# Performance work log

Measured on AMD Instinct MI355X. Metric: run time of the kernel, lower is better.

The kernel has to match this reference:

```python
import jax, jax.numpy as jnp
import numpy as np

DIM = 256
NUM_HEADS = 8
SAMPLE_RATIO = 4
B, H, W = 8, 32, 32
HEAD_DIM = DIM // NUM_HEADS
SCALE = HEAD_DIM ** (-0.5)


def conv1x1(x, w, b):
    # x: [B,C,H,W], w: [O,C], b: [O]  (1x1 conv == per-pixel channel matmul)
    return jnp.einsum('bchw,oc->bohw', x, w) + b[None, :, None, None]


def setup_inputs() -> dict:
    key = jax.random.key(0)
    ks = jax.random.split(key, 16)
    s = 0.02
    x = jax.random.normal(ks[0], (B, DIM, H, W), dtype=jnp.float32)
    # gumbel noise for the two gumbel-softmax gates (sampled once, fed as input)
    u_q = jax.random.uniform(ks[1], (B, SAMPLE_RATIO, H, W), minval=1e-6, maxval=1.0 - 1e-6)
    u_k = jax.random.uniform(ks[2], (B, SAMPLE_RATIO, H, W), minval=1e-6, maxval=1.0 - 1e-6)
    g_q = -jnp.log(-jnp.log(u_q))
    g_k = -jnp.log(-jnp.log(u_k))
    return {
        'x': x,
        'g_q': g_q,
        'g_k': g_k,
        'Wsq': jax.random.normal(ks[3], (SAMPLE_RATIO, DIM)) * s,
        'bsq': jnp.zeros((SAMPLE_RATIO,), jnp.float32),
        'Wsk': jax.random.normal(ks[4], (SAMPLE_RATIO, DIM)) * s,
        'bsk': jnp.zeros((SAMPLE_RATIO,), jnp.float32),
        'Wq': jax.random.normal(ks[5], (DIM, DIM)) * s,
        'bq': jnp.zeros((DIM,), jnp.float32),
        'Wk': jax.random.normal(ks[6], (DIM, DIM)) * s,
        'bk': jnp.zeros((DIM,), jnp.float32),
        'Wv': jax.random.normal(ks[7], (DIM, DIM)) * s,
        'bv': jnp.zeros((DIM,), jnp.float32),
        'Wp': jax.random.normal(ks[8], (DIM, DIM)) * s,
        'bp': jnp.zeros((DIM,), jnp.float32),
    }


def reference(x, g_q, g_k, Wsq, bsq, Wsk, bsk, Wq, bq, Wk, bk, Wv, bv, Wp, bp):
    Bn, C, Hh, Ww = x.shape
    N = Hh * Ww
    # gumbel-softmax (soft, tau=1) gates; keep channel 0 only
    sample_q = jax.nn.softmax(conv1x1(x, Wsq, bsq) + g_q, axis=1)[:, :1]   # [B,1,H,W]
    sample_k = jax.nn.softmax(conv1x1(x, Wsk, bsk) + g_k, axis=1)[:, :1]

    q = (sample_q * conv1x1(x, Wq, bq)).reshape(Bn, NUM_HEADS, HEAD_DIM, N)
    k = (sample_k * conv1x1(x, Wk, bk)).reshape(Bn, NUM_HEADS, HEAD_DIM, N)
    v_full = conv1x1(x, Wv, bv)                                            # shortcut [B,C,H,W]
    v = v_full.reshape(Bn, NUM_HEADS, HEAD_DIM, N)

    # dense attention: scores [B,h,N,N]
    attn = jax.nn.softmax(jnp.einsum('bhdn,bhdm->bhnm', q * SCALE, k), axis=-1)
    out = jnp.einsum('bhnm,bhdm->bhdn', attn, v).reshape(Bn, C, Hh, Ww)

    gated = sample_q * out + (1.0 - sample_q) * v_full
    return conv1x1(gated, Wp, bp)
```

## Files before the change

kernel.cpp:

```cpp
#include <hip/hip_runtime.h>
#include <hip/hip_bf16.h>

typedef __hip_bfloat16 bf16;
typedef __attribute__((ext_vector_type(8))) short short8;
typedef __attribute__((ext_vector_type(4))) short sh4;
typedef __attribute__((ext_vector_type(4))) float f32x4;

static __device__ __forceinline__ float bf2f(bf16 h) { return __bfloat162float(h); }
static __device__ __forceinline__ short f2bfs(float f) {
    bf16 h = __float2bfloat16(f);
    return *reinterpret_cast<short*>(&h);
}
static __device__ __forceinline__ short8 cvt8(float4 a, float4 b) {
    short8 o;
    o[0] = f2bfs(a.x); o[1] = f2bfs(a.y); o[2] = f2bfs(a.z); o[3] = f2bfs(a.w);
    o[4] = f2bfs(b.x); o[5] = f2bfs(b.y); o[6] = f2bfs(b.z); o[7] = f2bfs(b.w);
    return o;
}

constexpr int Bn = 8;
constexpr int C  = 256;
constexpr int N  = 1024;
constexpr int NH = 8;
constexpr int HD = 32;
constexpr int TS = 264;
constexpr float SCALE = 0.17677669529663687f;

__global__ void k_fused(
    const float* __restrict__ x, const float* __restrict__ gq, const float* __restrict__ gk,
    const float* __restrict__ Wsq, const float* __restrict__ bsq,
    const float* __restrict__ Wsk, const float* __restrict__ bsk,
    const float* __restrict__ Wq, const float* __restrict__ bq,
    const float* __restrict__ Wk, const float* __restrict__ bk,
    const float* __restrict__ Wv, const float* __restrict__ bv,
    const float* __restrict__ Wp,
    bf16* __restrict__ qo, bf16* __restrict__ ko, bf16* __restrict__ vo,
    bf16* __restrict__ Wpb, float* __restrict__ sqg)
{
    const int bx  = blockIdx.x;
    const int tid = threadIdx.x;

    if (bx >= 256) {
        const int seg = bx - 256;
        short* dst = reinterpret_cast<short*>(Wpb);
#pragma unroll
        for (int i = 0; i < 16; ++i) {
            int f4 = seg * 4096 + i * 256 + tid;
            float4 v = reinterpret_cast<const float4*>(Wp)[f4];
            sh4 o;
            o[0] = f2bfs(v.x); o[1] = f2bfs(v.y); o[2] = f2bfs(v.z); o[3] = f2bfs(v.w);
            *reinterpret_cast<sh4*>(dst + (size_t)f4 * 4) = o;
        }
        return;
    }

    __shared__ short T[32 * TS];
    __shared__ float sq_lds[32];
    __shared__ float sk_lds[32];

    const int wave = tid >> 6;
    const int lane = tid & 63;
    const int col  = lane & 15;
    const int quad = lane >> 4;

    const int b  = bx >> 5;
    const int n0 = (bx & 31) * 32;

    {
        const float* xp = x + (size_t)b * C * N + n0;
        const int row = tid >> 3;
        const int f   = tid & 7;
#pragma unroll
        for (int p = 0; p < 8; ++p) {
            int c = p * 32 + row;
            float4 v = *reinterpret_cast<const float4*>(xp + (size_t)c * N + f * 4);
            T[(f * 4 + 0) * TS + c] = f2bfs(v.x);
            T[(f * 4 + 1) * TS + c] = f2bfs(v.y);
            T[(f * 4 + 2) * TS + c] = f2bfs(v.z);
            T[(f * 4 + 3) * TS + c] = f2bfs(v.w);
        }
    }
    __syncthreads();

    if (wave == 0) {
        const float* wsrc = (col < 4) ? (Wsq + col * C) : (Wsk + (col & 3) * C);
        f32x4 ga[2] = {};
#pragma unroll
        for (int k0 = 0; k0 < 256; k0 += 32) {
            float4 w0 = *reinterpret_cast<const float4*>(wsrc + k0 + quad * 8);
            float4 w1 = *reinterpret_cast<const float4*>(wsrc + k0 + quad * 8 + 4);
            short8 af = cvt8(w0, w1);
            short8 b0 = *reinterpret_cast<const short8*>(&T[col * TS + k0 + quad * 8]);
            short8 b1 = *reinterpret_cast<const short8*>(&T[(16 + col) * TS + k0 + quad * 8]);
            ga[0] = __builtin_amdgcn_mfma_f32_16x16x32_bf16(af, b0, ga[0], 0, 0, 0);
            ga[1] = __builtin_amdgcn_mfma_f32_16x16x32_bf16(af, b1, ga[1], 0, 0, 0);
        }
        if (quad < 2) {
            const float* bsrc = (quad == 0) ? bsq : bsk;
            const float* gsrc = (quad == 0) ? gq : gk;
#pragma unroll
            for (int cf = 0; cf < 2; ++cf) {
                int n = n0 + cf * 16 + col;
                float a[4];
#pragma unroll
                for (int r = 0; r < 4; ++r)
                    a[r] = ga[cf][r] + bsrc[r] + gsrc[(size_t)b * 4 * N + (size_t)r * N + n];
                float mx = fmaxf(fmaxf(a[0], a[1]), fmaxf(a[2], a[3]));
                float e = 0.f;
#pragma unroll
                for (int r = 0; r < 4; ++r) e += __expf(a[r] - mx);
                float p0 = __expf(a[0] - mx) / e;
                if (quad == 0) { sq_lds[cf * 16 + col] = p0; sqg[b * N + n] = p0; }
                else            sk_lds[cf * 16 + col] = p0;
            }
        }
    }
    __syncthreads();

#pragma unroll
    for (int half = 0; half < 2; ++half) {
        const int mbase = wave * 192 + half * 96;
        f32x4 acc[6][2] = {};
#pragma unroll
        for (int k0 = 0; k0 < 256; k0 += 32) {
            short8 b0 = *reinterpret_cast<const short8*>(&T[col * TS + k0 + quad * 8]);
            short8 b1 = *reinterpret_cast<const short8*>(&T[(16 + col) * TS + k0 + quad * 8]);
#pragma unroll
            for (int i = 0; i < 6; ++i) {
                int m = mbase + i * 16;
                const float* wsrc = (m < 256) ? Wq : (m < 512) ? Wk : Wv;
                const float* wr = wsrc + (size_t)((m & 255) + col) * 256 + k0 + quad * 8;
                float4 w0 = *reinterpret_cast<const float4*>(wr);
                float4 w1 = *reinterpret_cast<const float4*>(wr + 4);
                short8 af = cvt8(w0, w1);
                acc[i][0] = __builtin_amdgcn_mfma_f32_16x16x32_bf16(af, b0, acc[i][0], 0, 0, 0);
                acc[i][1] = __builtin_amdgcn_mfma_f32_16x16x32_bf16(af, b1, acc[i][1], 0, 0, 0);
            }
        }
#pragma unroll
        for (int i = 0; i < 6; ++i) {
            int m = mbase + i * 16;
            int mat = m >> 8;
            int cr  = (m & 255) + quad * 4;
            const float* bb = (mat == 0) ? bq : (mat == 1) ? bk : bv;
            float bias[4];
#pragma unroll
            for (int r = 0; r < 4; ++r) bias[r] = bb[cr + r];
            if (mat < 2) {
                short* op = reinterpret_cast<short*>((mat == 0) ? qo : ko) + (size_t)b * N * C;
#pragma unroll
                for (int cf = 0; cf < 2; ++cf) {
                    int n = n0 + cf * 16 + col;
                    float g = (mat == 0) ? sq_lds[cf * 16 + col] * SCALE
                                         : sk_lds[cf * 16 + col];
                    sh4 pack;
#pragma unroll
                    for (int r = 0; r < 4; ++r) pack[r] = f2bfs((acc[i][cf][r] + bias[r]) * g);
                    *reinterpret_cast<sh4*>(op + (size_t)n * C + cr) = pack;
                }
            } else {
                bf16* op = vo + (size_t)b * C * N;
#pragma unroll
                for (int cf = 0; cf < 2; ++cf) {
                    int n = n0 + cf * 16 + col;
#pragma unroll
                    for (int r = 0; r < 4; ++r)
                        op[(size_t)(cr + r) * N + n] = __float2bfloat16(acc[i][cf][r] + bias[r]);
                }
            }
        }
    }
}

union SharedK2 {
    short P[4][32 * 72];
    short G[32 * TS];
};

__global__ void k_attnproj(
    const bf16* __restrict__ qo, const bf16* __restrict__ ko,
    const bf16* __restrict__ vo, const float* __restrict__ sqg,
    const bf16* __restrict__ Wpb, const float* __restrict__ bp,
    float* __restrict__ out)
{
    __shared__ SharedK2 sh;
    const int tid  = threadIdx.x;
    const int wave = tid >> 6;
    const int lane = tid & 63;
    const int col  = lane & 15;
    const int quad = lane >> 4;

    const int b  = blockIdx.x >> 5;
    const int n0 = (blockIdx.x & 31) * 32;

    const short* qbase = reinterpret_cast<const short*>(qo) + (size_t)b * N * C;
    const short* kbase_p = reinterpret_cast<const short*>(ko) + (size_t)b * N * C;
    const short* vbase = reinterpret_cast<const short*>(vo) + (size_t)b * C * N;

    float l[2][2] = {};
    f32x4 oac[2][2][2] = {};
    short* P = sh.P[wave];

#pragma unroll
    for (int hh = 0; hh < 2; ++hh) {
        const int h = wave * 2 + hh;
        const short* kp = kbase_p + h * HD + quad * 8;
        const short* vp = vbase + (size_t)h * HD * N;

        short8 qf[2];
#pragma unroll
        for (int g = 0; g < 2; ++g)
            qf[g] = *reinterpret_cast<const short8*>(qbase + (size_t)(n0 + g * 16 + col) * C + h * HD + quad * 8);

        short8 kf[4];
#pragma unroll
        for (int c = 0; c < 4; ++c)
            kf[c] = *reinterpret_cast<const short8*>(kp + (size_t)(c * 16 + col) * C);

        for (int kb = 0; kb < N; kb += 64) {
            short8 vf[2][2];
#pragma unroll
            for (int kg = 0; kg < 2; ++kg)
#pragma unroll
                for (int dh = 0; dh < 2; ++dh)
                    vf[kg][dh] = *reinterpret_cast<const short8*>(vp + (size_t)(dh * 16 + col) * N + kb + kg * 32 + quad * 8);

#pragma unroll
            for (int g = 0; g < 2; ++g) {
                float s[16];
#pragma unroll
                for (int c = 0; c < 4; ++c) {
                    f32x4 acc = {};
                    acc = __builtin_amdgcn_mfma_f32_16x16x32_bf16(kf[c], qf[g], acc, 0, 0, 0);
#pragma unroll
                    for (int r = 0; r < 4; ++r) s[c * 4 + r] = acc[r];
                }
                float p[16], lloc = 0.f;
#pragma unroll
                for (int i = 0; i < 16; ++i) { p[i] = __expf(s[i]); lloc += p[i]; }
                lloc += __shfl_xor(lloc, 16, 64);
                lloc += __shfl_xor(lloc, 32, 64);
                l[hh][g] += lloc;
#pragma unroll
                for (int c = 0; c < 4; ++c) {
                    sh4 pk;
#pragma unroll
                    for (int r = 0; r < 4; ++r) pk[r] = f2bfs(p[c * 4 + r]);
                    *reinterpret_cast<sh4*>(&P[(g * 16 + col) * 72 + c * 16 + quad * 4]) = pk;
                }
            }

            const int kn = (kb + 64) & (N - 1);
#pragma unroll
            for (int c = 0; c < 4; ++c)
                kf[c] = *reinterpret_cast<const short8*>(kp + (size_t)(kn + c * 16 + col) * C);

#pragma unroll
            for (int kg = 0; kg < 2; ++kg) {
#pragma unroll
                for (int g = 0; g < 2; ++g) {
                    short8 pf = *reinterpret_cast<const short8*>(&P[(g * 16 + col) * 72 + kg * 32 + quad * 8]);
#pragma unroll
                    for (int dh = 0; dh < 2; ++dh)
                        oac[hh][g][dh] = __builtin_amdgcn_mfma_f32_16x16x32_bf16(vf[kg][dh], pf, oac[hh][g][dh], 0, 0, 0);
                }
            }
        }
    }

    __syncthreads();

#pragma unroll
    for (int hh = 0; hh < 2; ++hh) {
        const int h = wave * 2 + hh;
        const short* vp = reinterpret_cast<const short*>(vbase) + (size_t)h * HD * N;
#pragma unroll
        for (int g = 0; g < 2; ++g) {
            const int q = n0 + g * 16 + col;
            const float invl = 1.f / l[hh][g];
            const float sqv  = sqg[b * N + q];
            const float hv   = 1.f - sqv;
#pragma unroll
            for (int dh = 0; dh < 2; ++dh) {
                sh4 pack;
#pragma unroll
                for (int r = 0; r < 4; ++r) {
                    int d = dh * 16 + quad * 4 + r;
                    float vb = bf2f(*reinterpret_cast<const bf16*>(vp + (size_t)d * N + q));
                    pack[r] = f2bfs(sqv * (oac[hh][g][dh][r] * invl) + hv * vb);
                }
                *reinterpret_cast<sh4*>(&sh.G[(g * 16 + col) * TS + h * HD + dh * 16 + quad * 4]) = pack;
            }
        }
    }

    __syncthreads();

    const short* Wm = reinterpret_cast<const short*>(Wpb);
    f32x4 pacc[4][2] = {};
#pragma unroll
    for (int k0 = 0; k0 < 256; k0 += 32) {
        short8 b0 = *reinterpret_cast<const short8*>(&sh.G[col * TS + k0 + quad * 8]);
        short8 b1 = *reinterpret_cast<const short8*>(&sh.G[(16 + col) * TS + k0 + quad * 8]);
#pragma unroll
        for (int i = 0; i < 4; ++i) {
            short8 af = *reinterpret_cast<const short8*>(Wm + (size_t)(wave * 64 + i * 16 + col) * 256 + k0 + quad * 8);
            pacc[i][0] = __builtin_amdgcn_mfma_f32_16x16x32_bf16(af, b0, pacc[i][0], 0, 0, 0);
            pacc[i][1] = __builtin_amdgcn_mfma_f32_16x16x32_bf16(af, b1, pacc[i][1], 0, 0, 0);
        }
    }
    float* op = out + (size_t)b * C * N;
#pragma unroll
    for (int i = 0; i < 4; ++i) {
        int cr = wave * 64 + i * 16 + quad * 4;
        float bias[4];
#pragma unroll
        for (int r = 0; r < 4; ++r) bias[r] = bp[cr + r];
#pragma unroll
        for (int cf = 0; cf < 2; ++cf) {
            int n = n0 + cf * 16 + col;
#pragma unroll
            for (int r = 0; r < 4; ++r)
                op[(size_t)(cr + r) * N + n] = pacc[i][cf][r] + bias[r];
        }
    }
}

extern "C" void kernel_launch(void* const* d_in, const int* in_sizes, int n_in,
                              void* d_out, int out_size, void* d_ws, size_t ws_size,
                              hipStream_t stream)
{
    const float* x   = (const float*)d_in[0];
    const float* gq  = (const float*)d_in[1];
    const float* gk  = (const float*)d_in[2];
    const float* Wsq = (const float*)d_in[3];
    const float* bsq = (const float*)d_in[4];
    const float* Wsk = (const float*)d_in[5];
    const float* bsk = (const float*)d_in[6];
    const float* Wq  = (const float*)d_in[7];
    const float* bq  = (const float*)d_in[8];
    const float* Wk  = (const float*)d_in[9];
    const float* bk  = (const float*)d_in[10];
    const float* Wv  = (const float*)d_in[11];
    const float* bv  = (const float*)d_in[12];
    const float* Wp  = (const float*)d_in[13];
    const float* bp  = (const float*)d_in[14];

    char* ws = (char*)d_ws;
    float* sqg = (float*)ws;
    bf16* Wpb  = (bf16*)(ws + 32768);
    bf16* qo   = (bf16*)(ws + 163840);
    bf16* ko   = qo + (size_t)Bn * N * C;
    bf16* vo   = ko + (size_t)Bn * N * C;
    float* out = (float*)d_out;

    k_fused<<<260, 256, 0, stream>>>(x, gq, gk, Wsq, bsq, Wsk, bsk,
                                     Wq, bq, Wk, bk, Wv, bv, Wp,
                                     qo, ko, vo, Wpb, sqg);
    k_attnproj<<<256, 256, 0, stream>>>(qo, ko, vo, sqg, Wpb, bp, out);
}
```

Before: 167.7 us.

## Double grid size in both kernels to fill more compute units

```diff
diff --git a/kernel.cpp b/kernel.cpp
--- a/kernel.cpp
+++ b/kernel.cpp
@@ -26,7 +26,7 @@
 constexpr int TS = 264;
 constexpr float SCALE = 0.17677669529663687f;
 
-__global__ void k_fused(
+__global__ __launch_bounds__(256) void k_fused2(
     const float* __restrict__ x, const float* __restrict__ gq, const float* __restrict__ gk,
     const float* __restrict__ Wsq, const float* __restrict__ bsq,
     const float* __restrict__ Wsk, const float* __restrict__ bsk,
@@ -40,8 +40,8 @@
     const int bx  = blockIdx.x;
     const int tid = threadIdx.x;
 
-    if (bx >= 256) {
-        const int seg = bx - 256;
+    if (bx >= 512) {
+        const int seg = bx - 512;
         short* dst = reinterpret_cast<short*>(Wpb);
 #pragma unroll
         for (int i = 0; i < 16; ++i) {
@@ -63,8 +63,10 @@
     const int col  = lane & 15;
     const int quad = lane >> 4;
 
-    const int b  = bx >> 5;
-    const int n0 = (bx & 31) * 32;
+    const int b     = bx >> 6;
+    const int tile  = (bx & 63) >> 1;
+    const int mhalf = bx & 1;
+    const int n0    = tile * 32;
 
     {
         const float* xp = x + (size_t)b * C * N + n0;
@@ -110,74 +112,75 @@
 #pragma unroll
                 for (int r = 0; r < 4; ++r) e += __expf(a[r] - mx);
                 float p0 = __expf(a[0] - mx) / e;
-                if (quad == 0) { sq_lds[cf * 16 + col] = p0; sqg[b * N + n] = p0; }
-                else            sk_lds[cf * 16 + col] = p0;
+                if (quad == 0) {
+                    sq_lds[cf * 16 + col] = p0;
+                    if (mhalf == 0) sqg[b * N + n] = p0;
+                } else {
+                    sk_lds[cf * 16 + col] = p0;
+                }
             }
         }
     }
     __syncthreads();
 
-#pragma unroll
-    for (int half = 0; half < 2; ++half) {
-        const int mbase = wave * 192 + half * 96;
-        f32x4 acc[6][2] = {};
-#pragma unroll
-        for (int k0 = 0; k0 < 256; k0 += 32) {
-            short8 b0 = *reinterpret_cast<const short8*>(&T[col * TS + k0 + quad * 8]);
-            short8 b1 = *reinterpret_cast<const short8*>(&T[(16 + col) * TS + k0 + quad * 8]);
-#pragma unroll
-            for (int i = 0; i < 6; ++i) {
-                int m = mbase + i * 16;
-                const float* wsrc = (m < 256) ? Wq : (m < 512) ? Wk : Wv;
-                const float* wr = wsrc + (size_t)((m & 255) + col) * 256 + k0 + quad * 8;
-                float4 w0 = *reinterpret_cast<const float4*>(wr);
-                float4 w1 = *reinterpret_cast<const float4*>(wr + 4);
-                short8 af = cvt8(w0, w1);
-                acc[i][0] = __builtin_amdgcn_mfma_f32_16x16x32_bf16(af, b0, acc[i][0], 0, 0, 0);
-                acc[i][1] = __builtin_amdgcn_mfma_f32_16x16x32_bf16(af, b1, acc[i][1], 0, 0, 0);
-            }
-        }
+    const int mbase = mhalf * 384 + wave * 96;
+    f32x4 acc[6][2] = {};
+#pragma unroll
+    for (int k0 = 0; k0 < 256; k0 += 32) {
+        short8 b0 = *reinterpret_cast<const short8*>(&T[col * TS + k0 + quad * 8]);
+        short8 b1 = *reinterpret_cast<const short8*>(&T[(16 + col) * TS + k0 + quad * 8]);
 #pragma unroll
         for (int i = 0; i < 6; ++i) {
             int m = mbase + i * 16;
-            int mat = m >> 8;
-            int cr  = (m & 255) + quad * 4;
-            const float* bb = (mat == 0) ? bq : (mat == 1) ? bk : bv;
-            float bias[4];
-#pragma unroll
-            for (int r = 0; r < 4; ++r) bias[r] = bb[cr + r];
-            if (mat < 2) {
-                short* op = reinterpret_cast<short*>((mat == 0) ? qo : ko) + (size_t)b * N * C;
-#pragma unroll
-                for (int cf = 0; cf < 2; ++cf) {
-                    int n = n0 + cf * 16 + col;
-                    float g = (mat == 0) ? sq_lds[cf * 16 + col] * SCALE
-                                         : sk_lds[cf * 16 + col];
-                    sh4 pack;
-#pragma unroll
-                    for (int r = 0; r < 4; ++r) pack[r] = f2bfs((acc[i][cf][r] + bias[r]) * g);
-                    *reinterpret_cast<sh4*>(op + (size_t)n * C + cr) = pack;
-                }
-            } else {
-                bf16* op = vo + (size_t)b * C * N;
-#pragma unroll
-                for (int cf = 0; cf < 2; ++cf) {
-                    int n = n0 + cf * 16 + col;
-#pragma unroll
-                    for (int r = 0; r < 4; ++r)
-                        op[(size_t)(cr + r) * N + n] = __float2bfloat16(acc[i][cf][r] + bias[r]);
-                }
+            const float* wsrc = (m < 256) ? Wq : (m < 512) ? Wk : Wv;
+            const float* wr = wsrc + (size_t)((m & 255) + col) * 256 + k0 + quad * 8;
+            float4 w0 = *reinterpret_cast<const float4*>(wr);
+            float4 w1 = *reinterpret_cast<const float4*>(wr + 4);
+            short8 af = cvt8(w0, w1);
+            acc[i][0] = __builtin_amdgcn_mfma_f32_16x16x32_bf16(af, b0, acc[i][0], 0, 0, 0);
+            acc[i][1] = __builtin_amdgcn_mfma_f32_16x16x32_bf16(af, b1, acc[i][1], 0, 0, 0);
+        }
+    }
+#pragma unroll
+    for (int i = 0; i < 6; ++i) {
+        int m = mbase + i * 16;
+        int mat = m >> 8;
+        int cr  = (m & 255) + quad * 4;
+        const float* bb = (mat == 0) ? bq : (mat == 1) ? bk : bv;
+        float bias[4];
+#pragma unroll
+        for (int r = 0; r < 4; ++r) bias[r] = bb[cr + r];
+        if (mat < 2) {
+            short* op = reinterpret_cast<short*>((mat == 0) ? qo : ko) + (size_t)b * N * C;
+#pragma unroll
+            for (int cf = 0; cf < 2; ++cf) {
+                int n = n0 + cf * 16 + col;
+                float g = (mat == 0) ? sq_lds[cf * 16 + col] * SCALE
+                                     : sk_lds[cf * 16 + col];
+                sh4 pack;
+#pragma unroll
+                for (int r = 0; r < 4; ++r) pack[r] = f2bfs((acc[i][cf][r] + bias[r]) * g);
+                *reinterpret_cast<sh4*>(op + (size_t)n * C + cr) = pack;
+            }
+        } else {
+            bf16* op = vo + (size_t)b * C * N;
+#pragma unroll
+            for (int cf = 0; cf < 2; ++cf) {
+                int n = n0 + cf * 16 + col;
+#pragma unroll
+                for (int r = 0; r < 4; ++r)
+                    op[(size_t)(cr + r) * N + n] = __float2bfloat16(acc[i][cf][r] + bias[r]);
             }
         }
     }
 }
 
 union SharedK2 {
-    short P[4][32 * 72];
-    short G[32 * TS];
+    short P[4][16 * 72];
+    short G[16 * TS];
 };
 
-__global__ void k_attnproj(
+__global__ __launch_bounds__(256) void k_attnproj2(
     const bf16* __restrict__ qo, const bf16* __restrict__ ko,
     const bf16* __restrict__ vo, const float* __restrict__ sqg,
     const bf16* __restrict__ Wpb, const float* __restrict__ bp,
@@ -190,15 +193,15 @@
     const int col  = lane & 15;
     const int quad = lane >> 4;
 
-    const int b  = blockIdx.x >> 5;
-    const int n0 = (blockIdx.x & 31) * 32;
-
-    const short* qbase = reinterpret_cast<const short*>(qo) + (size_t)b * N * C;
+    const int b  = blockIdx.x >> 6;
+    const int n0 = (blockIdx.x & 63) * 16;
+
+    const short* qbase   = reinterpret_cast<const short*>(qo) + (size_t)b * N * C;
     const short* kbase_p = reinterpret_cast<const short*>(ko) + (size_t)b * N * C;
-    const short* vbase = reinterpret_cast<const short*>(vo) + (size_t)b * C * N;
-
-    float l[2][2] = {};
-    f32x4 oac[2][2][2] = {};
+    const short* vbase   = reinterpret_cast<const short*>(vo) + (size_t)b * C * N;
+
+    float l[2] = {};
+    f32x4 oac[2][2] = {};
     short* P = sh.P[wave];
 
 #pragma unroll
@@ -207,10 +210,8 @@
         const short* kp = kbase_p + h * HD + quad * 8;
         const short* vp = vbase + (size_t)h * HD * N;
 
-        short8 qf[2];
-#pragma unroll
-        for (int g = 0; g < 2; ++g)
-            qf[g] = *reinterpret_cast<const short8*>(qbase + (size_t)(n0 + g * 16 + col) * C + h * HD + quad * 8);
+        short8 qf = *reinterpret_cast<const short8*>(
+            qbase + (size_t)(n0 + col) * C + h * HD + quad * 8);
 
         short8 kf[4];
 #pragma unroll
@@ -225,29 +226,26 @@
                 for (int dh = 0; dh < 2; ++dh)
                     vf[kg][dh] = *reinterpret_cast<const short8*>(vp + (size_t)(dh * 16 + col) * N + kb + kg * 32 + quad * 8);
 
-#pragma unroll
-            for (int g = 0; g < 2; ++g) {
-                float s[16];
-#pragma unroll
-                for (int c = 0; c < 4; ++c) {
-                    f32x4 acc = {};
-                    acc = __builtin_amdgcn_mfma_f32_16x16x32_bf16(kf[c], qf[g], acc, 0, 0, 0);
-#pragma unroll
-                    for (int r = 0; r < 4; ++r) s[c * 4 + r] = acc[r];
-                }
-                float p[16], lloc = 0.f;
-#pragma unroll
-                for (int i = 0; i < 16; ++i) { p[i] = __expf(s[i]); lloc += p[i]; }
-                lloc += __shfl_xor(lloc, 16, 64);
-                lloc += __shfl_xor(lloc, 32, 64);
-                l[hh][g] += lloc;
-#pragma unroll
-                for (int c = 0; c < 4; ++c) {
-                    sh4 pk;
-#pragma unroll
-                    for (int r = 0; r < 4; ++r) pk[r] = f2bfs(p[c * 4 + r]);
-                    *reinterpret_cast<sh4*>(&P[(g * 16 + col) * 72 + c * 16 + quad * 4]) = pk;
-                }
+            float s[16];
+#pragma unroll
+            for (int c = 0; c < 4; ++c) {
+                f32x4 acc = {};
+                acc = __builtin_amdgcn_mfma_f32_16x16x32_bf16(kf[c], qf, acc, 0, 0, 0);
+#pragma unroll
+                for (int r = 0; r < 4; ++r) s[c * 4 + r] = acc[r];
+            }
+            float p[16], lloc = 0.f;
+#pragma unroll
+            for (int i = 0; i < 16; ++i) { p[i] = __expf(s[i]); lloc += p[i]; }
+            lloc += __shfl_xor(lloc, 16, 64);
+            lloc += __shfl_xor(lloc, 32, 64);
+            l[hh] += lloc;
+#pragma unroll
+            for (int c = 0; c < 4; ++c) {
+                sh4 pk;
+#pragma unroll
+                for (int r = 0; r < 4; ++r) pk[r] = f2bfs(p[c * 4 + r]);
+                *reinterpret_cast<sh4*>(&P[col * 72 + c * 16 + quad * 4]) = pk;
             }
 
             const int kn = (kb + 64) & (N - 1);
@@ -257,29 +255,25 @@
 
 #pragma unroll
             for (int kg = 0; kg < 2; ++kg) {
-#pragma unroll
-                for (int g = 0; g < 2; ++g) {
-                    short8 pf = *reinterpret_cast<const short8*>(&P[(g * 16 + col) * 72 + kg * 32 + quad * 8]);
-#pragma unroll
-                    for (int dh = 0; dh < 2; ++dh)
-                        oac[hh][g][dh] = __builtin_amdgcn_mfma_f32_16x16x32_bf16(vf[kg][dh], pf, oac[hh][g][dh], 0, 0, 0);
-                }
+                short8 pf = *reinterpret_cast<const short8*>(&P[col * 72 + kg * 32 + quad * 8]);
+#pragma unroll
+                for (int dh = 0; dh < 2; ++dh)
+                    oac[hh][dh] = __builtin_amdgcn_mfma_f32_16x16x32_bf16(vf[kg][dh], pf, oac[hh][dh], 0, 0, 0);
             }
         }
     }
 
     __syncthreads();
 
-#pragma unroll
-    for (int hh = 0; hh < 2; ++hh) {
-        const int h = wave * 2 + hh;
-        const short* vp = reinterpret_cast<const short*>(vbase) + (size_t)h * HD * N;
-#pragma unroll
-        for (int g = 0; g < 2; ++g) {
-            const int q = n0 + g * 16 + col;
-            const float invl = 1.f / l[hh][g];
-            const float sqv  = sqg[b * N + q];
-            const float hv   = 1.f - sqv;
+    {
+        const int q = n0 + col;
+        const float sqv  = sqg[b * N + q];
+        const float hv   = 1.f - sqv;
+#pragma unroll
+        for (int hh = 0; hh < 2; ++hh) {
+            const int h = wave * 2 + hh;
+            const short* vp = vbase + (size_t)h * HD * N;
+            const float invl = 1.f / l[hh];
 #pragma unroll
             for (int dh = 0; dh < 2; ++dh) {
                 sh4 pack;
@@ -287,9 +281,9 @@
                 for (int r = 0; r < 4; ++r) {
                     int d = dh * 16 + quad * 4 + r;
                     float vb = bf2f(*reinterpret_cast<const bf16*>(vp + (size_t)d * N + q));
-                    pack[r] = f2bfs(sqv * (oac[hh][g][dh][r] * invl) + hv * vb);
+                    pack[r] = f2bfs(sqv * (oac[hh][dh][r] * invl) + hv * vb);
                 }
-                *reinterpret_cast<sh4*>(&sh.G[(g * 16 + col) * TS + h * HD + dh * 16 + quad * 4]) = pack;
+                *reinterpret_cast<sh4*>(&sh.G[col * TS + h * HD + dh * 16 + quad * 4]) = pack;
             }
         }
     }
@@ -297,32 +291,23 @@
     __syncthreads();
 
     const short* Wm = reinterpret_cast<const short*>(Wpb);
-    f32x4 pacc[4][2] = {};
+    f32x4 pacc[4] = {};
 #pragma unroll
     for (int k0 = 0; k0 < 256; k0 += 32) {
         short8 b0 = *reinterpret_cast<const short8*>(&sh.G[col * TS + k0 + quad * 8]);
-        short8 b1 = *reinterpret_cast<const short8*>(&sh.G[(16 + col) * TS + k0 + quad * 8]);
 #pragma unroll
         for (int i = 0; i < 4; ++i) {
             short8 af = *reinterpret_cast<const short8*>(Wm + (size_t)(wave * 64 + i * 16 + col) * 256 + k0 + quad * 8);
-            pacc[i][0] = __builtin_amdgcn_mfma_f32_16x16x32_bf16(af, b0, pacc[i][0], 0, 0, 0);
-            pacc[i][1] = __builtin_amdgcn_mfma_f32_16x16x32_bf16(af, b1, pacc[i][1], 0, 0, 0);
+            pacc[i] = __builtin_amdgcn_mfma_f32_16x16x32_bf16(af, b0, pacc[i], 0, 0, 0);
         }
     }
     float* op = out + (size_t)b * C * N;
 #pragma unroll
     for (int i = 0; i < 4; ++i) {
         int cr = wave * 64 + i * 16 + quad * 4;
-        float bias[4];
-#pragma unroll
-        for (int r = 0; r < 4; ++r) bias[r] = bp[cr + r];
-#pragma unroll
-        for (int cf = 0; cf < 2; ++cf) {
-            int n = n0 + cf * 16 + col;
-#pragma unroll
-            for (int r = 0; r < 4; ++r)
-                op[(size_t)(cr + r) * N + n] = pacc[i][cf][r] + bias[r];
-        }
+#pragma unroll
+        for (int r = 0; r < 4; ++r)
+            op[(size_t)(cr + r) * N + n0 + col] = pacc[i][r] + bp[cr + r];
     }
 }
 
@@ -354,8 +339,8 @@
     bf16* vo   = ko + (size_t)Bn * N * C;
     float* out = (float*)d_out;
 
-    k_fused<<<260, 256, 0, stream>>>(x, gq, gk, Wsq, bsq, Wsk, bsk,
-                                     Wq, bq, Wk, bk, Wv, bv, Wp,
-                                     qo, ko, vo, Wpb, sqg);
-    k_attnproj<<<256, 256, 0, stream>>>(qo, ko, vo, sqg, Wpb, bp, out);
-}
+    k_fused2<<<516, 256, 0, stream>>>(x, gq, gk, Wsq, bsq, Wsk, bsk,
+                                      Wq, bq, Wk, bk, Wv, bv, Wp,
+                                      qo, ko, vo, Wpb, sqg);
+    k_attnproj2<<<512, 256, 0, stream>>>(qo, ko, vo, sqg, Wpb, bp, out);
+}
```

Measured after the change: 184.3 us. 1.1x slower.
